# Performance work log

Measured on AMD Instinct MI355X. Metric: run time of the kernel, lower is better.

The kernel has to match this reference:

```python
import jax, jax.numpy as jnp
import numpy as np

DIM = 1024
BATCH = 16384
NUM_LAYERS = 6
S_E = 0.1   # strength_entail
S_C = 0.1   # strength_contra
S_N = 0.05  # strength_neutral
S_NB = 0.05 # strength_neutral_boost
EPS = 1e-12


def _normalize(x, axis=-1):
    # matches F.normalize: x / max(||x||, eps)
    n = jnp.sqrt(jnp.sum(x * x, axis=axis, keepdims=True))
    return x / jnp.maximum(n, EPS)


def setup_inputs() -> dict:
    key = jax.random.key(0)
    ks = jax.random.split(key, 8)
    return {
        "h0": jax.random.normal(ks[0], (BATCH, DIM), dtype=jnp.float32),
        "W1": jax.random.normal(ks[1], (DIM, DIM), dtype=jnp.float32) * 0.02,
        "b1": jnp.zeros((DIM,), dtype=jnp.float32),
        "W2": jax.random.normal(ks[2], (DIM, DIM), dtype=jnp.float32) * 0.02,
        "b2": jnp.zeros((DIM,), dtype=jnp.float32),
        "anchor_entail": jax.random.normal(ks[3], (DIM,), dtype=jnp.float32),
        "anchor_contra": jax.random.normal(ks[4], (DIM,), dtype=jnp.float32),
        "anchor_neutral": jax.random.normal(ks[5], (DIM,), dtype=jnp.float32),
    }


def reference(h0, W1, b1, W2, b2, anchor_entail, anchor_contra, anchor_neutral):
    # Static collapse with three fixed anchors (rot_rank=0, adaptive_metric=False).
    e_dir = _normalize(anchor_entail, axis=0)   # [D]
    c_dir = _normalize(anchor_contra, axis=0)
    n_dir = _normalize(anchor_neutral, axis=0)

    h = h0
    for _ in range(NUM_LAYERS):
        h_n = _normalize(h)                      # [B, D]
        a_e = h_n @ e_dir                        # [B]
        a_c = h_n @ c_dir
        a_n = h_n @ n_dir
        # divergence_from_alignment: div = 1 - align
        div_e = 1.0 - a_e
        div_c = 1.0 - a_c
        div_n = 1.0 - a_n

        # small MLP update: Linear -> Tanh -> Linear (torch Linear: x @ W.T + b)
        delta = jnp.tanh(h @ W1.T + b1) @ W2.T + b2

        # per-anchor force directions: normalize(h - anchor_dir)
        f_e = _normalize(h - e_dir)
        f_c = _normalize(h - c_dir)
        f_n = _normalize(h - n_dir)

        # boundary_proximity(a_e, a_c): 1 when equidistant from E and C
        boundary = jnp.clip(1.0 - jnp.abs(a_e - a_c), 0.0, 1.0)  # [B]

        h = (h + delta
             - S_E * div_e[:, None] * f_e
             - S_C * div_c[:, None] * f_c
             - S_N * div_n[:, None] * f_n
             - S_NB * boundary[:, None] * f_n)

        # norm clamp at 10 (soft rescale, as in the torch code)
        h_norm = jnp.sqrt(jnp.sum(h * h, axis=-1, keepdims=True))
        h = jnp.where(h_norm > 10.0, h * (10.0 / (h_norm + 1e-8)), h)
    return h
```

## Files before the change

kernel.cpp:

```cpp
#include <hip/hip_runtime.h>
#include <hip/hip_bf16.h>
#include <math.h>

#define DIM 1024
#define BATCH 16384
#define NLAYER 6

typedef __bf16 bf16_t;
typedef __attribute__((ext_vector_type(8))) __bf16 bf16x8;
typedef __attribute__((ext_vector_type(4))) float f32x4;

__device__ __forceinline__ void gload16(const void* g, void* l) {
  __builtin_amdgcn_global_load_lds(
      (const __attribute__((address_space(1))) void*)g,
      (__attribute__((address_space(3))) void*)l, 16, 0, 0);
}

__device__ __forceinline__ float fast_tanh(float x) {
  x = fminf(9.f, fmaxf(-9.f, x));
  const float e = __expf(x + x);
  return (e - 1.f) * __builtin_amdgcn_rcpf(e + 1.f);
}

__device__ __forceinline__ float bf2f(unsigned short u) {
  return __uint_as_float(((unsigned int)u) << 16);
}

template <int MODE>
__global__ __launch_bounds__(256, 4) void gemm_kernel(
    const bf16_t* __restrict__ A, const bf16_t* __restrict__ W,
    const float* __restrict__ bias, bf16_t* __restrict__ outB,
    float* __restrict__ outF, const f32x4* __restrict__ coef,
    const f32x4* __restrict__ colpack, const float* __restrict__ scaleArr,
    const bf16_t* __restrict__ hbIn, float* __restrict__ part) {
  __shared__ __align__(16) bf16_t sA[128 * 64];
  __shared__ __align__(16) bf16_t sB[128 * 64];
  const int tid = threadIdx.x;
  const int w = tid >> 6;
  const int lane = tid & 63;
  const int bm = blockIdx.x * 128;
  const int bn = blockIdx.y * 128;
  const int byi = blockIdx.y;
  const int wm = (w & 1) * 64;
  const int wn = (w >> 1) * 64;
  const int lm = lane & 15;
  const int lc = lane >> 4;

  f32x4 acc[4][4] = {};

  const int srow = tid >> 3;
  const int swz = ((tid & 7) ^ (srow & 7)) * 8;
  const bf16_t* gA = A + (size_t)(bm + srow) * DIM + swz;
  const bf16_t* gW = W + (size_t)(bn + srow) * DIM + swz;
  char* lA = (char*)sA + w * 1024;
  char* lB = (char*)sB + w * 1024;

  for (int kt = 0; kt < DIM; kt += 64) {
#pragma unroll
    for (int q = 0; q < 4; ++q) {
      gload16(gA + kt + (size_t)q * 32 * DIM, lA + q * 4096);
      gload16(gW + kt + (size_t)q * 32 * DIM, lB + q * 4096);
    }
    __syncthreads();
#pragma unroll
    for (int kh = 0; kh < 2; ++kh) {
      bf16x8 aF[4], bF[4];
      const int lgc = kh * 4 + lc;
#pragma unroll
      for (int i = 0; i < 4; ++i) {
        const int rowA = wm + i * 16 + lm;
        aF[i] = *(const bf16x8*)((char*)sA + rowA * 128 +
                                 ((lgc ^ (lm & 7)) << 4));
      }
#pragma unroll
      for (int j = 0; j < 4; ++j) {
        const int rowB = wn + j * 16 + lm;
        bF[j] = *(const bf16x8*)((char*)sB + rowB * 128 +
                                 ((lgc ^ (lm & 7)) << 4));
      }
#pragma unroll
      for (int i = 0; i < 4; ++i)
#pragma unroll
        for (int j = 0; j < 4; ++j)
          acc[i][j] = __builtin_amdgcn_mfma_f32_16x16x32_bf16(
              aF[i], bF[j], acc[i][j], 0, 0, 0);
    }
    __syncthreads();
  }

  const int r0 = lc << 2;
#pragma unroll
  for (int i = 0; i < 4; ++i) {
    const int rowBase = bm + wm + i * 16 + r0;
    if constexpr (MODE == 0) {
      float s4[4];
#pragma unroll
      for (int r = 0; r < 4; ++r) s4[r] = scaleArr[rowBase + r];
#pragma unroll
      for (int j = 0; j < 4; ++j) {
        const int col = bn + wn + j * 16 + lm;
        const float bv = bias[col];
#pragma unroll
        for (int r = 0; r < 4; ++r)
          outB[(size_t)(rowBase + r) * DIM + col] =
              (bf16_t)fast_tanh(s4[r] * acc[i][j][r] + bv);
      }
    } else {
      f32x4 cf[4];
#pragma unroll
      for (int r = 0; r < 4; ++r) cf[r] = coef[rowBase + r];
      float ss[4] = {}, de[4] = {}, dc[4] = {}, dn[4] = {};
#pragma unroll
      for (int j = 0; j < 4; ++j) {
        const int col = bn + wn + j * 16 + lm;
        const f32x4 cp = colpack[col];
#pragma unroll
        for (int r = 0; r < 4; ++r) {
          const size_t idx = (size_t)(rowBase + r) * DIM + col;
          const float hp = (float)hbIn[idx];
          const float v = acc[i][j][r] + cp.w + cf[r].x * cp.x +
                          cf[r].y * cp.y + cf[r].z * cp.z + cf[r].w * hp;
          if constexpr (MODE == 1) outB[idx] = (bf16_t)v;
          if constexpr (MODE == 2) outF[idx] = v;
          ss[r] += v * v;
          de[r] += v * cp.x;
          dc[r] += v * cp.y;
          dn[r] += v * cp.z;
        }
      }
      const int slot = byi * 2 + (w >> 1);
#pragma unroll
      for (int r = 0; r < 4; ++r) {
        float a = ss[r], b = de[r], c = dc[r], d = dn[r];
#pragma unroll
        for (int mask = 1; mask < 16; mask <<= 1) {
          a += __shfl_xor(a, mask);
          b += __shfl_xor(b, mask);
          c += __shfl_xor(c, mask);
          d += __shfl_xor(d, mask);
        }
        if (lm == 0) {
          f32x4 o;
          o.x = a; o.y = b; o.z = c; o.w = d;
          ((f32x4*)part)[(size_t)(rowBase + r) * 16 + slot] = o;
        }
      }
    }
  }
}

__global__ __launch_bounds__(256) void convert_kernel(
    const float* __restrict__ part, f32x4* __restrict__ coef,
    float* __restrict__ scaleArr) {
  const int row = blockIdx.x * 256 + threadIdx.x;
  const f32x4* p = (const f32x4*)part + (size_t)row * 16;
  float S = 0.f, E = 0.f, C = 0.f, N = 0.f;
#pragma unroll
  for (int b = 0; b < 16; ++b) {
    const f32x4 v = p[b];
    S += v.x; E += v.y; C += v.z; N += v.w;
  }
  const float norm = sqrtf(S);
  float scale = 1.f;
  if (norm > 10.f) scale = 10.f / (norm + 1e-8f);
  const float invn = 1.f / fmaxf(norm, 1e-12f);
  const float ae = E * invn;
  const float ac = C * invn;
  const float an = N * invn;
  const float nc = norm * scale;
  const float re = sqrtf(fmaxf(nc * nc - 2.f * nc * ae + 1.f, 0.f));
  const float rc = sqrtf(fmaxf(nc * nc - 2.f * nc * ac + 1.f, 0.f));
  const float rn = sqrtf(fmaxf(nc * nc - 2.f * nc * an + 1.f, 0.f));
  const float boundary = fminf(fmaxf(1.f - fabsf(ae - ac), 0.f), 1.f);
  f32x4 cf;
  cf.x = 0.1f * (1.f - ae) / fmaxf(re, 1e-12f);
  cf.y = 0.1f * (1.f - ac) / fmaxf(rc, 1e-12f);
  cf.z = (0.05f * (1.f - an) + 0.05f * boundary) / fmaxf(rn, 1e-12f);
  cf.w = scale * (1.f - cf.x - cf.y - cf.z);
  coef[row] = cf;
  scaleArr[row] = scale;
}

__global__ __launch_bounds__(256) void stats0_kernel(
    const float* __restrict__ src, bf16_t* __restrict__ dstb,
    float* __restrict__ scaleArr, f32x4* __restrict__ coef,
    const float* __restrict__ dirs) {
  const int row = blockIdx.x;
  const int t = threadIdx.x;
  const float4 v = ((const float4*)src)[(size_t)row * 256 + t];
  const float4 e = ((const float4*)dirs)[t];
  const float4 c = ((const float4*)dirs)[t + 256];
  const float4 n = ((const float4*)dirs)[t + 512];
  float ss = v.x * v.x + v.y * v.y + v.z * v.z + v.w * v.w;
  float de = v.x * e.x + v.y * e.y + v.z * e.z + v.w * e.w;
  float dc = v.x * c.x + v.y * c.y + v.z * c.z + v.w * c.w;
  float dn = v.x * n.x + v.y * n.y + v.z * n.z + v.w * n.w;
#pragma unroll
  for (int off = 32; off; off >>= 1) {
    ss += __shfl_down(ss, off);
    de += __shfl_down(de, off);
    dc += __shfl_down(dc, off);
    dn += __shfl_down(dn, off);
  }
  __shared__ float red[4][4];
  const int w = t >> 6;
  if ((t & 63) == 0) {
    red[w][0] = ss; red[w][1] = de; red[w][2] = dc; red[w][3] = dn;
  }
  __syncthreads();
  union { bf16_t b[4]; uint2 u; } pk;
  pk.b[0] = (bf16_t)v.x; pk.b[1] = (bf16_t)v.y;
  pk.b[2] = (bf16_t)v.z; pk.b[3] = (bf16_t)v.w;
  ((uint2*)dstb)[(size_t)row * 256 + t] = pk.u;
  if (t == 0) {
    float S = 0, E = 0, C = 0, N = 0;
#pragma unroll
    for (int i = 0; i < 4; ++i) {
      S += red[i][0]; E += red[i][1]; C += red[i][2]; N += red[i][3];
    }
    const float norm = sqrtf(S);
    const float scale = 1.f;
    const float invn = 1.f / fmaxf(norm, 1e-12f);
    const float ae = E * invn;
    const float ac = C * invn;
    const float an = N * invn;
    const float nc = norm * scale;
    const float re = sqrtf(fmaxf(nc * nc - 2.f * nc * ae + 1.f, 0.f));
    const float rc = sqrtf(fmaxf(nc * nc - 2.f * nc * ac + 1.f, 0.f));
    const float rn = sqrtf(fmaxf(nc * nc - 2.f * nc * an + 1.f, 0.f));
    const float boundary = fminf(fmaxf(1.f - fabsf(ae - ac), 0.f), 1.f);
    f32x4 cf;
    cf.x = 0.1f * (1.f - ae) / fmaxf(re, 1e-12f);
    cf.y = 0.1f * (1.f - ac) / fmaxf(rc, 1e-12f);
    cf.z = (0.05f * (1.f - an) + 0.05f * boundary) / fmaxf(rn, 1e-12f);
    cf.w = scale * (1.f - cf.x - cf.y - cf.z);
    coef[row] = cf;
    scaleArr[row] = scale;
  }
}

__global__ __launch_bounds__(256) void finalize_kernel(
    float* __restrict__ outF, const float* __restrict__ scaleArr) {
  const int row = blockIdx.x;
  const int t = threadIdx.x;
  const float s = scaleArr[row];
  float4 v = ((float4*)outF)[(size_t)row * 256 + t];
  v.x *= s; v.y *= s; v.z *= s; v.w *= s;
  ((float4*)outF)[(size_t)row * 256 + t] = v;
}

__global__ __launch_bounds__(256) void prep_dirs(
    const float* __restrict__ ae, const float* __restrict__ ac,
    const float* __restrict__ an, float* __restrict__ dirs) {
  const int t = threadIdx.x;
  const float4 a = ((const float4*)ae)[t];
  const float4 b = ((const float4*)ac)[t];
  const float4 c = ((const float4*)an)[t];
  float sa = a.x * a.x + a.y * a.y + a.z * a.z + a.w * a.w;
  float sb = b.x * b.x + b.y * b.y + b.z * b.z + b.w * b.w;
  float sc = c.x * c.x + c.y * c.y + c.z * c.z + c.w * c.w;
#pragma unroll
  for (int off = 32; off; off >>= 1) {
    sa += __shfl_down(sa, off);
    sb += __shfl_down(sb, off);
    sc += __shfl_down(sc, off);
  }
  __shared__ float red[4][3];
  __shared__ float fin[3];
  const int w = t >> 6;
  if ((t & 63) == 0) { red[w][0] = sa; red[w][1] = sb; red[w][2] = sc; }
  __syncthreads();
  if (t == 0) {
    float x = 0, y = 0, z = 0;
#pragma unroll
    for (int i = 0; i < 4; ++i) { x += red[i][0]; y += red[i][1]; z += red[i][2]; }
    fin[0] = x; fin[1] = y; fin[2] = z;
  }
  __syncthreads();
  const float ia = 1.f / fmaxf(sqrtf(fin[0]), 1e-12f);
  const float ib = 1.f / fmaxf(sqrtf(fin[1]), 1e-12f);
  const float ic = 1.f / fmaxf(sqrtf(fin[2]), 1e-12f);
  float4 oa, ob, oc;
  oa.x = a.x * ia; oa.y = a.y * ia; oa.z = a.z * ia; oa.w = a.w * ia;
  ob.x = b.x * ib; ob.y = b.y * ib; ob.z = b.z * ib; ob.w = b.w * ib;
  oc.x = c.x * ic; oc.y = c.y * ic; oc.z = c.z * ic; oc.w = c.w * ic;
  ((float4*)dirs)[t] = oa;
  ((float4*)dirs)[t + 256] = ob;
  ((float4*)dirs)[t + 512] = oc;
}

__global__ __launch_bounds__(256) void prep_cols(
    const float* __restrict__ dirs, const float* __restrict__ b2,
    f32x4* __restrict__ colpack) {
  const int t = threadIdx.x;
  const float4 e = ((const float4*)dirs)[t];
  const float4 c = ((const float4*)dirs)[t + 256];
  const float4 n = ((const float4*)dirs)[t + 512];
  const float4 b = ((const float4*)b2)[t];
  f32x4 o;
  o.x = e.x; o.y = c.x; o.z = n.x; o.w = b.x; colpack[4 * t + 0] = o;
  o.x = e.y; o.y = c.y; o.z = n.y; o.w = b.y; colpack[4 * t + 1] = o;
  o.x = e.z; o.y = c.z; o.z = n.z; o.w = b.z; colpack[4 * t + 2] = o;
  o.x = e.w; o.y = c.w; o.z = n.w; o.w = b.w; colpack[4 * t + 3] = o;
}

__global__ __launch_bounds__(256) void cast_w_kernel(
    const float* __restrict__ W, bf16_t* __restrict__ Wb) {
  const int i = blockIdx.x * 256 + threadIdx.x;
  const float4 v = ((const float4*)W)[i];
  union { bf16_t b[4]; uint2 u; } pk;
  pk.b[0] = (bf16_t)v.x; pk.b[1] = (bf16_t)v.y;
  pk.b[2] = (bf16_t)v.z; pk.b[3] = (bf16_t)v.w;
  ((uint2*)Wb)[i] = pk.u;
}

extern "C" void kernel_launch(void* const* d_in, const int* in_sizes, int n_in,
                              void* d_out, int out_size, void* d_ws,
                              size_t ws_size, hipStream_t stream) {
  const float* h0 = (const float*)d_in[0];
  const float* W1 = (const float*)d_in[1];
  const float* b1 = (const float*)d_in[2];
  const float* W2 = (const float*)d_in[3];
  const float* b2 = (const float*)d_in[4];
  const float* ae = (const float*)d_in[5];
  const float* ac = (const float*)d_in[6];
  const float* an = (const float*)d_in[7];
  float* outF = (float*)d_out;

  char* ws = (char*)d_ws;
  bf16_t* hb = (bf16_t*)ws;  ws += (size_t)BATCH * DIM * 2;
  bf16_t* Tb = (bf16_t*)ws;  ws += (size_t)BATCH * DIM * 2;
  bf16_t* W1b = (bf16_t*)ws; ws += (size_t)DIM * DIM * 2;
  bf16_t* W2b = (bf16_t*)ws; ws += (size_t)DIM * DIM * 2;
  float* dirs = (float*)ws;  ws += 3 * DIM * 4;
  f32x4* colpack = (f32x4*)ws; ws += DIM * 16;
  f32x4* coef = (f32x4*)ws;  ws += (size_t)BATCH * 16;
  float* scaleArr = (float*)ws; ws += (size_t)BATCH * 4;
  float* part = (float*)ws;  ws += (size_t)BATCH * 16 * 16;

  prep_dirs<<<1, 256, 0, stream>>>(ae, ac, an, dirs);
  prep_cols<<<1, 256, 0, stream>>>(dirs, b2, colpack);
  cast_w_kernel<<<DIM * DIM / 1024, 256, 0, stream>>>(W1, W1b);
  cast_w_kernel<<<DIM * DIM / 1024, 256, 0, stream>>>(W2, W2b);
  stats0_kernel<<<BATCH, 256, 0, stream>>>(h0, hb, scaleArr, coef, dirs);

  dim3 grid(BATCH / 128, DIM / 128);
  for (int l = 0; l < NLAYER; ++l) {
    gemm_kernel<0><<<grid, 256, 0, stream>>>(hb, W1b, b1, Tb, nullptr, nullptr,
                                             nullptr, scaleArr, nullptr,
                                             nullptr);
    if (l < NLAYER - 1) {
      gemm_kernel<1><<<grid, 256, 0, stream>>>(Tb, W2b, b2, hb, nullptr, coef,
                                               colpack, nullptr, hb, part);
      convert_kernel<<<BATCH / 256, 256, 0, stream>>>(part, coef, scaleArr);
    } else {
      gemm_kernel<2><<<grid, 256, 0, stream>>>(Tb, W2b, b2, nullptr, outF, coef,
                                               colpack, nullptr, hb, part);
      convert_kernel<<<BATCH / 256, 256, 0, stream>>>(part, coef, scaleArr);
      finalize_kernel<<<BATCH, 256, 0, stream>>>(outF, scaleArr);
    }
  }
}
```

Baseline: 763.6 us.

## Load GEMM fragments directly from global memory and remap blocks per XCD

Drops the LDS staging and the barriers in the GEMM. Each wave now loads its MFMA A/B fragments straight from global memory into registers, with the k-loop unrolled by 4. Blocks are launched on a 1D grid and remapped so that blocks sharing an A row-panel land on the same XCD, which should improve L2 reuse. Without LDS sharing, every wave fetches its fragments separately, so global and L2 traffic goes up. The lower occupancy hint (4 to 3) makes room for the extra registers.

```diff
diff --git a/kernel.cpp b/kernel.cpp
--- a/kernel.cpp
+++ b/kernel.cpp
@@ -9,12 +9,6 @@
 typedef __bf16 bf16_t;
 typedef __attribute__((ext_vector_type(8))) __bf16 bf16x8;
 typedef __attribute__((ext_vector_type(4))) float f32x4;
-
-__device__ __forceinline__ void gload16(const void* g, void* l) {
-  __builtin_amdgcn_global_load_lds(
-      (const __attribute__((address_space(1))) void*)g,
-      (__attribute__((address_space(3))) void*)l, 16, 0, 0);
-}
 
 __device__ __forceinline__ float fast_tanh(float x) {
   x = fminf(9.f, fmaxf(-9.f, x));
@@ -27,20 +21,22 @@
 }
 
 template <int MODE>
-__global__ __launch_bounds__(256, 4) void gemm_kernel(
+__global__ __launch_bounds__(256, 3) void gemm_kernel(
     const bf16_t* __restrict__ A, const bf16_t* __restrict__ W,
     const float* __restrict__ bias, bf16_t* __restrict__ outB,
     float* __restrict__ outF, const f32x4* __restrict__ coef,
     const f32x4* __restrict__ colpack, const float* __restrict__ scaleArr,
     const bf16_t* __restrict__ hbIn, float* __restrict__ part) {
-  __shared__ __align__(16) bf16_t sA[128 * 64];
-  __shared__ __align__(16) bf16_t sB[128 * 64];
   const int tid = threadIdx.x;
   const int w = tid >> 6;
   const int lane = tid & 63;
-  const int bm = blockIdx.x * 128;
-  const int bn = blockIdx.y * 128;
-  const int byi = blockIdx.y;
+  const int id = blockIdx.x;
+  const int xcd = id & 7;
+  const int j_ = id >> 3;
+  const int bxi = (xcd << 4) + (j_ >> 3);
+  const int byi = j_ & 7;
+  const int bm = bxi * 128;
+  const int bn = byi * 128;
   const int wm = (w & 1) * 64;
   const int wn = (w >> 1) * 64;
   const int lm = lane & 15;
@@ -48,44 +44,32 @@
 
   f32x4 acc[4][4] = {};
 
-  const int srow = tid >> 3;
-  const int swz = ((tid & 7) ^ (srow & 7)) * 8;
-  const bf16_t* gA = A + (size_t)(bm + srow) * DIM + swz;
-  const bf16_t* gW = W + (size_t)(bn + srow) * DIM + swz;
-  char* lA = (char*)sA + w * 1024;
-  char* lB = (char*)sB + w * 1024;
-
+  const bf16_t* pa = A + (size_t)(bm + wm + lm) * DIM + lc * 8;
+  const bf16_t* pb = W + (size_t)(bn + wn + lm) * DIM + lc * 8;
+
+#pragma unroll 4
   for (int kt = 0; kt < DIM; kt += 64) {
-#pragma unroll
-    for (int q = 0; q < 4; ++q) {
-      gload16(gA + kt + (size_t)q * 32 * DIM, lA + q * 4096);
-      gload16(gW + kt + (size_t)q * 32 * DIM, lB + q * 4096);
-    }
-    __syncthreads();
-#pragma unroll
-    for (int kh = 0; kh < 2; ++kh) {
-      bf16x8 aF[4], bF[4];
-      const int lgc = kh * 4 + lc;
-#pragma unroll
-      for (int i = 0; i < 4; ++i) {
-        const int rowA = wm + i * 16 + lm;
-        aF[i] = *(const bf16x8*)((char*)sA + rowA * 128 +
-                                 ((lgc ^ (lm & 7)) << 4));
-      }
-#pragma unroll
-      for (int j = 0; j < 4; ++j) {
-        const int rowB = wn + j * 16 + lm;
-        bF[j] = *(const bf16x8*)((char*)sB + rowB * 128 +
-                                 ((lgc ^ (lm & 7)) << 4));
-      }
-#pragma unroll
-      for (int i = 0; i < 4; ++i)
-#pragma unroll
-        for (int j = 0; j < 4; ++j)
+    bf16x8 aF[4][2], bF[4][2];
+#pragma unroll
+    for (int i = 0; i < 4; ++i)
+#pragma unroll
+      for (int kh = 0; kh < 2; ++kh)
+        aF[i][kh] =
+            *(const bf16x8*)(pa + (size_t)i * 16 * DIM + kt + kh * 32);
+#pragma unroll
+    for (int j = 0; j < 4; ++j)
+#pragma unroll
+      for (int kh = 0; kh < 2; ++kh)
+        bF[j][kh] =
+            *(const bf16x8*)(pb + (size_t)j * 16 * DIM + kt + kh * 32);
+#pragma unroll
+    for (int i = 0; i < 4; ++i)
+#pragma unroll
+      for (int j = 0; j < 4; ++j)
+#pragma unroll
+        for (int kh = 0; kh < 2; ++kh)
           acc[i][j] = __builtin_amdgcn_mfma_f32_16x16x32_bf16(
-              aF[i], bF[j], acc[i][j], 0, 0, 0);
-    }
-    __syncthreads();
+              aF[i][kh], bF[j][kh], acc[i][j], 0, 0, 0);
   }
 
   const int r0 = lc << 2;
@@ -344,7 +328,7 @@
   cast_w_kernel<<<DIM * DIM / 1024, 256, 0, stream>>>(W2, W2b);
   stats0_kernel<<<BATCH, 256, 0, stream>>>(h0, hb, scaleArr, coef, dirs);
 
-  dim3 grid(BATCH / 128, DIM / 128);
+  const int grid = (BATCH / 128) * (DIM / 128);
   for (int l = 0; l < NLAYER; ++l) {
     gemm_kernel<0><<<grid, 256, 0, stream>>>(hb, W1b, b1, Tb, nullptr, nullptr,
                                              nullptr, scaleArr, nullptr,
```

Measured after the change: 1.684 ms. 2.21x slower.

## Double-buffer GEMM K-tiles with async LDS loads overlapping MFMA compute

Applied to the files above, without the earlier changes.

The GEMM main loop goes from single-buffered 64-wide K tiles to double-buffered 32-wide K tiles. The next tile's global-to-LDS loads are issued before computing the current one, with a partial vmcnt wait so memory latency overlaps MFMA work. The LDS swizzle layout is reworked to fit the 32-wide tiles. In exchange there are twice as many barriers per K, and smaller tiles per iteration with manual waitcnt/sched_barrier control that could be fragile.

```diff
diff --git a/kernel.cpp b/kernel.cpp
--- a/kernel.cpp
+++ b/kernel.cpp
@@ -33,8 +33,8 @@
     float* __restrict__ outF, const f32x4* __restrict__ coef,
     const f32x4* __restrict__ colpack, const float* __restrict__ scaleArr,
     const bf16_t* __restrict__ hbIn, float* __restrict__ part) {
-  __shared__ __align__(16) bf16_t sA[128 * 64];
-  __shared__ __align__(16) bf16_t sB[128 * 64];
+  __shared__ __align__(16) bf16_t sA[2][128 * 32];
+  __shared__ __align__(16) bf16_t sB[2][128 * 32];
   const int tid = threadIdx.x;
   const int w = tid >> 6;
   const int lane = tid & 63;
@@ -48,45 +48,62 @@
 
   f32x4 acc[4][4] = {};
 
-  const int srow = tid >> 3;
-  const int swz = ((tid & 7) ^ (srow & 7)) * 8;
-  const bf16_t* gA = A + (size_t)(bm + srow) * DIM + swz;
-  const bf16_t* gW = W + (size_t)(bn + srow) * DIM + swz;
-  char* lA = (char*)sA + w * 1024;
-  char* lB = (char*)sB + w * 1024;
-
-  for (int kt = 0; kt < DIM; kt += 64) {
-#pragma unroll
-    for (int q = 0; q < 4; ++q) {
-      gload16(gA + kt + (size_t)q * 32 * DIM, lA + q * 4096);
-      gload16(gW + kt + (size_t)q * 32 * DIM, lB + q * 4096);
-    }
-    __syncthreads();
-#pragma unroll
-    for (int kh = 0; kh < 2; ++kh) {
-      bf16x8 aF[4], bF[4];
-      const int lgc = kh * 4 + lc;
-#pragma unroll
-      for (int i = 0; i < 4; ++i) {
-        const int rowA = wm + i * 16 + lm;
-        aF[i] = *(const bf16x8*)((char*)sA + rowA * 128 +
-                                 ((lgc ^ (lm & 7)) << 4));
-      }
-#pragma unroll
-      for (int j = 0; j < 4; ++j) {
-        const int rowB = wn + j * 16 + lm;
-        bF[j] = *(const bf16x8*)((char*)sB + rowB * 128 +
-                                 ((lgc ^ (lm & 7)) << 4));
-      }
-#pragma unroll
-      for (int i = 0; i < 4; ++i)
-#pragma unroll
-        for (int j = 0; j < 4; ++j)
-          acc[i][j] = __builtin_amdgcn_mfma_f32_16x16x32_bf16(
-              aF[i], bF[j], acc[i][j], 0, 0, 0);
-    }
-    __syncthreads();
-  }
+  const int rp = lane >> 3;
+  const int phys = lane & 7;
+  const int log8 = phys ^ rp;
+  const int ghalf = log8 >> 2;
+  const int gch = log8 & 3;
+  const int rowp0 = 8 * w + rp;
+  const bf16_t* gA0 = A + (size_t)(bm + rowp0 + ghalf * 64) * DIM + gch * 8;
+  const bf16_t* gW0 = W + (size_t)(bn + rowp0 + ghalf * 64) * DIM + gch * 8;
+
+#define STAGE(buf, koff)                                                   \
+  {                                                                        \
+    char* dA_ = (char*)&sA[(buf)][0] + w * 1024;                           \
+    char* dB_ = (char*)&sB[(buf)][0] + w * 1024;                           \
+    gload16(gA0 + (koff), dA_);                                            \
+    gload16(gA0 + (koff) + (size_t)32 * DIM, dA_ + 4096);                  \
+    gload16(gW0 + (koff), dB_);                                            \
+    gload16(gW0 + (koff) + (size_t)32 * DIM, dB_ + 4096);                  \
+  }
+
+  const int aOff = lm * 128 + (((((wm >> 6) << 2) + lc) ^ (lm & 7)) << 4);
+  const int bOff = lm * 128 + (((((wn >> 6) << 2) + lc) ^ (lm & 7)) << 4);
+
+#define TILE_COMPUTE(buf)                                                  \
+  {                                                                        \
+    const char* cA_ = (const char*)&sA[(buf)][0];                          \
+    const char* cB_ = (const char*)&sB[(buf)][0];                          \
+    bf16x8 aF[4], bF[4];                                                   \
+    _Pragma("unroll") for (int i = 0; i < 4; ++i)                          \
+        aF[i] = *(const bf16x8*)(cA_ + aOff + i * 2048);                   \
+    _Pragma("unroll") for (int j = 0; j < 4; ++j)                          \
+        bF[j] = *(const bf16x8*)(cB_ + bOff + j * 2048);                   \
+    _Pragma("unroll") for (int i = 0; i < 4; ++i)                          \
+        _Pragma("unroll") for (int j = 0; j < 4; ++j) acc[i][j] =          \
+            __builtin_amdgcn_mfma_f32_16x16x32_bf16(aF[i], bF[j],          \
+                                                    acc[i][j], 0, 0, 0);   \
+  }
+
+  STAGE(0, 0);
+  for (int t = 0; t < 31; ++t) {
+    STAGE((t + 1) & 1, (t + 1) * 32);
+    asm volatile("s_waitcnt vmcnt(4)" ::: "memory");
+    __builtin_amdgcn_sched_barrier(0);
+    __builtin_amdgcn_s_barrier();
+    __builtin_amdgcn_sched_barrier(0);
+    TILE_COMPUTE(t & 1);
+    __builtin_amdgcn_sched_barrier(0);
+    __builtin_amdgcn_s_barrier();
+    __builtin_amdgcn_sched_barrier(0);
+  }
+  asm volatile("s_waitcnt vmcnt(0)" ::: "memory");
+  __builtin_amdgcn_sched_barrier(0);
+  __builtin_amdgcn_s_barrier();
+  __builtin_amdgcn_sched_barrier(0);
+  TILE_COMPUTE(1);
+#undef STAGE
+#undef TILE_COMPUTE
 
   const int r0 = lc << 2;
 #pragma unroll
```

New measurement: 789.3 us. 1.03x slower.

## Rewrite GEMM as 256x256 tile with double-buffered LDS and staggered prefetch

Applied to the files above, without the earlier changes.

Replaces the 128x128 tile, 256-thread GEMM with a 256x256 tile and 8 waves, each wave computing 128x64. LDS becomes a 128KB double buffer for A and B. Global-to-LDS loads for later k-steps are interleaved with the MFMA phases, paced by explicit s_barrier, waitcnt and setprio. The intent is to overlap memory with compute and raise arithmetic intensity per block. The costs are fewer blocks (256 per GEMM), which may underfill the CUs, higher register pressure from 32 accumulators, and a fragile hand-written sync schedule.

```diff
diff --git a/kernel.cpp b/kernel.cpp
--- a/kernel.cpp
+++ b/kernel.cpp
@@ -27,83 +27,145 @@
 }
 
 template <int MODE>
-__global__ __launch_bounds__(256, 4) void gemm_kernel(
+__global__ __launch_bounds__(512, 2) void gemm_kernel(
     const bf16_t* __restrict__ A, const bf16_t* __restrict__ W,
     const float* __restrict__ bias, bf16_t* __restrict__ outB,
     float* __restrict__ outF, const f32x4* __restrict__ coef,
     const f32x4* __restrict__ colpack, const float* __restrict__ scaleArr,
     const bf16_t* __restrict__ hbIn, float* __restrict__ part) {
-  __shared__ __align__(16) bf16_t sA[128 * 64];
-  __shared__ __align__(16) bf16_t sB[128 * 64];
+  __shared__ __align__(16) char smem[131072];
   const int tid = threadIdx.x;
   const int w = tid >> 6;
   const int lane = tid & 63;
-  const int bm = blockIdx.x * 128;
-  const int bn = blockIdx.y * 128;
+  const int bm = blockIdx.x * 256;
+  const int bn = blockIdx.y * 256;
   const int byi = blockIdx.y;
-  const int wm = (w & 1) * 64;
-  const int wn = (w >> 1) * 64;
+  const int wm = w >> 2;
+  const int wn = w & 3;
   const int lm = lane & 15;
   const int lc = lane >> 4;
 
-  f32x4 acc[4][4] = {};
-
-  const int srow = tid >> 3;
-  const int swz = ((tid & 7) ^ (srow & 7)) * 8;
-  const bf16_t* gA = A + (size_t)(bm + srow) * DIM + swz;
-  const bf16_t* gW = W + (size_t)(bn + srow) * DIM + swz;
-  char* lA = (char*)sA + w * 1024;
-  char* lB = (char*)sB + w * 1024;
-
-  for (int kt = 0; kt < DIM; kt += 64) {
-#pragma unroll
-    for (int q = 0; q < 4; ++q) {
-      gload16(gA + kt + (size_t)q * 32 * DIM, lA + q * 4096);
-      gload16(gW + kt + (size_t)q * 32 * DIM, lB + q * 4096);
-    }
-    __syncthreads();
-#pragma unroll
-    for (int kh = 0; kh < 2; ++kh) {
-      bf16x8 aF[4], bF[4];
-      const int lgc = kh * 4 + lc;
-#pragma unroll
-      for (int i = 0; i < 4; ++i) {
-        const int rowA = wm + i * 16 + lm;
-        aF[i] = *(const bf16x8*)((char*)sA + rowA * 128 +
-                                 ((lgc ^ (lm & 7)) << 4));
-      }
-#pragma unroll
-      for (int j = 0; j < 4; ++j) {
-        const int rowB = wn + j * 16 + lm;
-        bF[j] = *(const bf16x8*)((char*)sB + rowB * 128 +
-                                 ((lgc ^ (lm & 7)) << 4));
-      }
-#pragma unroll
-      for (int i = 0; i < 4; ++i)
-#pragma unroll
-        for (int j = 0; j < 4; ++j)
-          acc[i][j] = __builtin_amdgcn_mfma_f32_16x16x32_bf16(
-              aF[i], bF[j], acc[i][j], 0, 0, 0);
-    }
-    __syncthreads();
-  }
+  f32x4 acc[8][4] = {};
+  bf16x8 Bf[4][2];
+
+  const int srow = lane >> 3;
+  const int swzl = ((lane & 7) ^ (srow & 7)) * 8;
+  const bf16_t* stA = A + (size_t)(bm + w * 16 + srow) * DIM + swzl;
+  const bf16_t* stB = W + (size_t)(bn + w * 16 + srow) * DIM + swzl;
+
+  int chOff[2];
+  chOff[0] = ((lc) ^ (lm & 7)) << 4;
+  chOff[1] = ((4 + lc) ^ (lm & 7)) << 4;
+  const int aBase0 = wm * 16384 + lm * 128;
+  const int bBase0 = 65536 + (wn >> 1) * 16384 + (wn & 1) * 8192 + lm * 128;
+
+#define STA(buf, half, ko)                                                  \
+  {                                                                         \
+    gload16(stA + (size_t)((half)*128) * DIM + (ko),                        \
+            smem + (buf)*32768 + (half)*16384 + w * 2048);                  \
+    gload16(stA + (size_t)((half)*128 + 8) * DIM + (ko),                    \
+            smem + (buf)*32768 + (half)*16384 + w * 2048 + 1024);           \
+  }
+#define STB(buf, half, ko)                                                  \
+  {                                                                         \
+    gload16(stB + (size_t)((half)*128) * DIM + (ko),                        \
+            smem + 65536 + (buf)*32768 + (half)*16384 + w * 2048);          \
+    gload16(stB + (size_t)((half)*128 + 8) * DIM + (ko),                    \
+            smem + 65536 + (buf)*32768 + (half)*16384 + w * 2048 + 1024);   \
+  }
+#define RDA(buf, f, kh) \
+  (*(const bf16x8*)(smem + (buf)*32768 + aBase0 + (f)*2048 + chOff[kh]))
+#define RDB(buf, j, kh) \
+  (*(const bf16x8*)(smem + (buf)*32768 + bBase0 + (j)*2048 + chOff[kh]))
+
+#define PH(buf, q, STG, VM)                                                 \
+  {                                                                         \
+    if ((q) == 0) {                                                         \
+      _Pragma("unroll") for (int j = 0; j < 4; ++j) {                       \
+        Bf[j][0] = RDB(buf, j, 0);                                          \
+        Bf[j][1] = RDB(buf, j, 1);                                          \
+      }                                                                     \
+    }                                                                       \
+    bf16x8 aA[2][2];                                                        \
+    aA[0][0] = RDA(buf, 2 * (q), 0);                                        \
+    aA[0][1] = RDA(buf, 2 * (q), 1);                                        \
+    aA[1][0] = RDA(buf, 2 * (q) + 1, 0);                                    \
+    aA[1][1] = RDA(buf, 2 * (q) + 1, 1);                                    \
+    STG;                                                                    \
+    __builtin_amdgcn_sched_barrier(0);                                      \
+    __builtin_amdgcn_s_barrier();                                           \
+    asm volatile("s_waitcnt lgkmcnt(0)" ::: "memory");                      \
+    __builtin_amdgcn_sched_barrier(0);                                      \
+    __builtin_amdgcn_s_setprio(1);                                          \
+    _Pragma("unroll") for (int s = 0; s < 2; ++s)                           \
+        _Pragma("unroll") for (int j = 0; j < 4; ++j)                       \
+            _Pragma("unroll") for (int kh = 0; kh < 2; ++kh)                \
+                acc[2 * (q) + s][j] =                                       \
+        __builtin_amdgcn_mfma_f32_16x16x32_bf16(aA[s][kh], Bf[j][kh],       \
+                                                acc[2 * (q) + s][j], 0, 0,  \
+                                                0);                         \
+    __builtin_amdgcn_s_setprio(0);                                          \
+    VM;                                                                     \
+    __builtin_amdgcn_sched_barrier(0);                                      \
+    __builtin_amdgcn_s_barrier();                                           \
+  }
+
+  STA(0, 0, 0);
+  STA(0, 1, 0);
+  STB(0, 0, 0);
+  STB(0, 1, 0);
+  STB(1, 0, 64);
+  STB(1, 1, 64);
+  asm volatile("s_waitcnt vmcnt(4)" ::: "memory");
+  __builtin_amdgcn_s_barrier();
+
+#pragma unroll 1
+  for (int i = 0; i < 7; ++i) {
+    const int kA1 = (2 * i + 1) * 64;
+    const int kN = (2 * i + 2) * 64;
+    const int kB1 = (2 * i + 3) * 64;
+    PH(0, 0, STA(1, 0, kA1), )
+    PH(0, 1, STA(1, 1, kA1), )
+    PH(0, 2, STB(0, 0, kN), )
+    PH(0, 3, STB(0, 1, kN),
+       asm volatile("s_waitcnt vmcnt(4)" ::: "memory"))
+    PH(1, 0, STA(0, 0, kN), )
+    PH(1, 1, STA(0, 1, kN), )
+    PH(1, 2, STB(1, 0, kB1), )
+    PH(1, 3, STB(1, 1, kB1),
+       asm volatile("s_waitcnt vmcnt(4)" ::: "memory"))
+  }
+  PH(0, 0, STA(1, 0, 15 * 64), )
+  PH(0, 1, STA(1, 1, 15 * 64), )
+  PH(0, 2, , )
+  PH(0, 3, , asm volatile("s_waitcnt vmcnt(0)" ::: "memory"))
+  PH(1, 0, , )
+  PH(1, 1, , )
+  PH(1, 2, , )
+  PH(1, 3, , )
+
+#undef STA
+#undef STB
+#undef RDA
+#undef RDB
+#undef PH
 
   const int r0 = lc << 2;
 #pragma unroll
-  for (int i = 0; i < 4; ++i) {
-    const int rowBase = bm + wm + i * 16 + r0;
+  for (int f = 0; f < 8; ++f) {
+    const int rowBase = bm + wm * 128 + f * 16 + r0;
     if constexpr (MODE == 0) {
       float s4[4];
 #pragma unroll
       for (int r = 0; r < 4; ++r) s4[r] = scaleArr[rowBase + r];
 #pragma unroll
       for (int j = 0; j < 4; ++j) {
-        const int col = bn + wn + j * 16 + lm;
+        const int col = bn + wn * 64 + j * 16 + lm;
         const float bv = bias[col];
 #pragma unroll
         for (int r = 0; r < 4; ++r)
           outB[(size_t)(rowBase + r) * DIM + col] =
-              (bf16_t)fast_tanh(s4[r] * acc[i][j][r] + bv);
+              (bf16_t)fast_tanh(s4[r] * acc[f][j][r] + bv);
       }
     } else {
       f32x4 cf[4];
@@ -112,13 +174,13 @@
       float ss[4] = {}, de[4] = {}, dc[4] = {}, dn[4] = {};
 #pragma unroll
       for (int j = 0; j < 4; ++j) {
-        const int col = bn + wn + j * 16 + lm;
+        const int col = bn + wn * 64 + j * 16 + lm;
         const f32x4 cp = colpack[col];
 #pragma unroll
         for (int r = 0; r < 4; ++r) {
           const size_t idx = (size_t)(rowBase + r) * DIM + col;
           const float hp = (float)hbIn[idx];
-          const float v = acc[i][j][r] + cp.w + cf[r].x * cp.x +
+          const float v = acc[f][j][r] + cp.w + cf[r].x * cp.x +
                           cf[r].y * cp.y + cf[r].z * cp.z + cf[r].w * hp;
           if constexpr (MODE == 1) outB[idx] = (bf16_t)v;
           if constexpr (MODE == 2) outF[idx] = v;
@@ -128,7 +190,7 @@
           dn[r] += v * cp.z;
         }
       }
-      const int slot = byi * 2 + (w >> 1);
+      const int slot = byi * 4 + wn;
 #pragma unroll
       for (int r = 0; r < 4; ++r) {
         float a = ss[r], b = de[r], c = dc[r], d = dn[r];
@@ -344,17 +406,17 @@
   cast_w_kernel<<<DIM * DIM / 1024, 256, 0, stream>>>(W2, W2b);
   stats0_kernel<<<BATCH, 256, 0, stream>>>(h0, hb, scaleArr, coef, dirs);
 
-  dim3 grid(BATCH / 128, DIM / 128);
+  dim3 grid(BATCH / 256, DIM / 256);
   for (int l = 0; l < NLAYER; ++l) {
-    gemm_kernel<0><<<grid, 256, 0, stream>>>(hb, W1b, b1, Tb, nullptr, nullptr,
+    gemm_kernel<0><<<grid, 512, 0, stream>>>(hb, W1b, b1, Tb, nullptr, nullptr,
                                              nullptr, scaleArr, nullptr,
                                              nullptr);
     if (l < NLAYER - 1) {
-      gemm_kernel<1><<<grid, 256, 0, stream>>>(Tb, W2b, b2, hb, nullptr, coef,
+      gemm_kernel<1><<<grid, 512, 0, stream>>>(Tb, W2b, b2, hb, nullptr, coef,
                                                colpack, nullptr, hb, part);
       convert_kernel<<<BATCH / 256, 256, 0, stream>>>(part, coef, scaleArr);
     } else {
-      gemm_kernel<2><<<grid, 256, 0, stream>>>(Tb, W2b, b2, nullptr, outF, coef,
+      gemm_kernel<2><<<grid, 512, 0, stream>>>(Tb, W2b, b2, nullptr, outF, coef,
                                                colpack, nullptr, hb, part);
       convert_kernel<<<BATCH / 256, 256, 0, stream>>>(part, coef, scaleArr);
       finalize_kernel<<<BATCH, 256, 0, stream>>>(outF, scaleArr);
```

Measured after the change: 688.8 us. -9.8%, faster.
